# Kernel tuning notes

Hardware: AMD Instinct MI355X
Metric: run time of the kernel (lower is better)

## Reference

```python
import jax, jax.numpy as jnp
import numpy as np

B, N, H, FE, M, PASSES, OUT = 512, 40, 128, 16, 128, 3, 128
NEG = -1e9


def setup_inputs() -> dict:
    key = jax.random.key(0)
    ks = jax.random.split(key, 16)
    am = jax.random.bernoulli(ks[0], 0.1, (B, N, N))
    am = (am | jnp.swapaxes(am, 1, 2)) & (~jnp.eye(N, dtype=bool))[None]
    edges = jax.random.uniform(ks[1], (B, N, N, FE), dtype=jnp.float32) * am[..., None].astype(jnp.float32)
    nodes = jax.random.normal(ks[2], (B, N, H), dtype=jnp.float32)
    s = lambda f: 1.0 / np.sqrt(f)
    return {
        "nodes": nodes,
        "edges": edges,
        "We": jax.random.normal(ks[3], (FE, M), dtype=jnp.float32) * s(FE),
        "Wn": jax.random.normal(ks[4], (H, M), dtype=jnp.float32) * s(H),
        "Wm": jax.random.normal(ks[5], (H, M), dtype=jnp.float32) * s(H),
        "Wi": jax.random.normal(ks[6], (M, 3 * H), dtype=jnp.float32) * s(M),
        "Wh": jax.random.normal(ks[7], (H, 3 * H), dtype=jnp.float32) * s(H),
        "bi": jnp.zeros((3 * H,), jnp.float32),
        "bh": jnp.zeros((3 * H,), jnp.float32),
        "Wg": jax.random.normal(ks[8], (2 * H, OUT), dtype=jnp.float32) * s(2 * H),
        "bg": jnp.zeros((OUT,), jnp.float32),
        "Wo": jax.random.normal(ks[9], (2 * H, OUT), dtype=jnp.float32) * s(2 * H),
        "bo": jnp.zeros((OUT,), jnp.float32),
    }


def _forward(nodes, edges, We, Wn, Wm, Wi, Wh, bi, bh, Wg, bg, Wo, bo):
    adj = jnp.sum(edges, axis=3)                      # (B,N,N)
    nghb_mask = adj > 0                               # neighbor exists
    node_mask = jnp.any(nghb_mask, axis=-1)           # (B,N) node has >=1 neighbor

    h = nodes                                         # hidden == input feature dim
    edge_proj = jnp.einsum("bijf,fm->bijm", edges, We)  # precompute, edges fixed
    for _ in range(PASSES):
        # attention energies over neighbors j of node i (masked softmax)
        nghb_proj = jnp.einsum("bjh,hm->bjm", h, Wn)  # (B,N,M)
        e = jnp.tanh(edge_proj + nghb_proj[:, None, :, :])        # (B,N,N,M)
        e = jnp.where(nghb_mask[..., None], e, NEG)
        att = jax.nn.softmax(e, axis=2)                            # over neighbor axis j
        emb = jnp.einsum("bjh,hm->bjm", h, Wm)                     # (B,N,M)
        messages = jnp.einsum("bijm,bjm->bim", att, emb)           # (B,N,M)
        # GRU cell update (only for existing nodes, as in the node-batch scatter)
        gi = messages @ Wi + bi
        gh = h @ Wh + bh
        r = jax.nn.sigmoid(gi[..., :H] + gh[..., :H])
        z = jax.nn.sigmoid(gi[..., H:2 * H] + gh[..., H:2 * H])
        n = jnp.tanh(gi[..., 2 * H:] + r * gh[..., 2 * H:])
        h_new = (1.0 - z) * n + z * h
        h = jnp.where(node_mask[..., None], h_new, h)

    # gated graph readout over existing nodes
    cat = jnp.concatenate([h, nodes], axis=-1)        # (B,N,2H)
    gate = jax.nn.sigmoid(cat @ Wg + bg)
    emb_out = cat @ Wo + bo
    out = jnp.sum(node_mask[..., None] * gate * emb_out, axis=1)   # (B,OUT)
    return out


def reference(nodes, edges, We, Wn, Wm, Wi, Wh, bi, bh, Wg, bg, Wo, bo):
    return _forward(nodes, edges, We, Wn, Wm, Wi, Wh, bi, bh, Wg, bg, Wo, bo)
```

## Files before the change

kernel.cpp:

```cpp
#include <hip/hip_runtime.h>

#define T 512
constexpr int Bc = 512, Nc = 40, Hc = 128, FEc = 16, Mc = 128, OUTc = 128, NPASS = 3;
constexpr int ROWP = 136;
constexpr int EPOOL = 512;

typedef __attribute__((ext_vector_type(8))) short short8;
typedef __attribute__((ext_vector_type(4))) float floatx4;
typedef __attribute__((ext_vector_type(4))) float fvec4;

constexpr int WS_WN = 0, WS_WM = 16384, WS_WI = 32768, WS_WH = 81920, WS_WG = 131072, WS_WO = 163840;

__device__ __forceinline__ float fast_rcp(float x) { return __builtin_amdgcn_rcpf(x); }
__device__ __forceinline__ float fast_sigmoid(float x) { return fast_rcp(1.f + __expf(-x)); }
__device__ __forceinline__ float fast_tanh(float x) {
    float t = __expf(2.f * x);
    return 1.f - 2.f * fast_rcp(t + 1.f);
}
__device__ __forceinline__ float bf2f(unsigned short u) {
    union { unsigned int i; float f; } v; v.i = ((unsigned int)u) << 16; return v.f;
}
__device__ __forceinline__ unsigned short f2bf(float f) {
    union { float f; unsigned int i; } v; v.f = f;
    unsigned int r = v.i + 0x7fff + ((v.i >> 16) & 1);
    return (unsigned short)(r >> 16);
}
__device__ __forceinline__ float bflo(unsigned int d) {
    union { unsigned int i; float f; } v; v.i = d << 16; return v.f;
}
__device__ __forceinline__ float bfhi(unsigned int d) {
    union { unsigned int i; float f; } v; v.i = d & 0xffff0000u; return v.f;
}

__device__ __forceinline__ floatx4 mm(short8 a, short8 b, floatx4 c) {
    return __builtin_amdgcn_mfma_f32_16x16x32_bf16(a, b, c, 0, 0, 0);
}
__device__ __forceinline__ short8 afrag(const unsigned short* buf, int mt, int kt, int lane) {
    int row = mt * 16 + (lane & 15); row = row > 39 ? 39 : row;
    return *(const short8*)(buf + row * ROWP + kt * 32 + (lane >> 4) * 8);
}
__device__ __forceinline__ short8 bfrag(const unsigned short* w, int nt, int nKT, int kt, int lane) {
    return *(const short8*)(w + ((nt * nKT + kt) * 64 + lane) * 8);
}

__global__ void prep_kernel(const float* __restrict__ Wn, const float* __restrict__ Wm,
                            const float* __restrict__ Wi, const float* __restrict__ Wh,
                            const float* __restrict__ Wg, const float* __restrict__ Wo,
                            unsigned short* __restrict__ ws) {
    int c = blockIdx.x, lane = threadIdx.x;
    int quad = lane >> 4, l16 = lane & 15;
    const float* W; int N, nKT, local; unsigned short* dst;
    if (c < 32)       { W = Wn; N = 128; nKT = 4; local = c;       dst = ws + WS_WN; }
    else if (c < 64)  { W = Wm; N = 128; nKT = 4; local = c - 32;  dst = ws + WS_WM; }
    else if (c < 160) { W = Wi; N = 384; nKT = 4; local = c - 64;  dst = ws + WS_WI; }
    else if (c < 256) { W = Wh; N = 384; nKT = 4; local = c - 160; dst = ws + WS_WH; }
    else if (c < 320) { W = Wg; N = 128; nKT = 8; local = c - 256; dst = ws + WS_WG; }
    else              { W = Wo; N = 128; nKT = 8; local = c - 320; dst = ws + WS_WO; }
    int nt = local / nKT, kt = local % nKT;
    short8 v;
#pragma unroll
    for (int j = 0; j < 8; ++j) {
        int k = kt * 32 + quad * 8 + j;
        v[j] = (short)f2bf(W[k * N + nt * 16 + l16]);
    }
    *(short8*)(dst + local * 512 + lane * 8) = v;
}

__global__ __launch_bounds__(T, 4) void mpnn_kernel(
    const float* __restrict__ nodes, const float* __restrict__ edges,
    const float* __restrict__ We, const float* __restrict__ bi,
    const float* __restrict__ bh, const float* __restrict__ bg,
    const float* __restrict__ bo, const unsigned short* __restrict__ ws,
    float* __restrict__ out)
{
    __shared__ __attribute__((aligned(16))) unsigned short s_hb[Nc * ROWP];
    __shared__ __attribute__((aligned(16))) unsigned short s_mb[Nc * ROWP];
    __shared__ __attribute__((aligned(16))) unsigned short s_npb[Nc * ROWP];
    __shared__ __attribute__((aligned(16))) unsigned short s_eb[Nc * ROWP];
    __shared__ __attribute__((aligned(16))) unsigned short s_pool[EPOOL * FEc];
    __shared__ unsigned char s_nbr[Nc][Nc];
    __shared__ int s_cnt[Nc];
    __shared__ int s_off[Nc];
    __shared__ int s_total;

    const int b = blockIdx.x, tid = threadIdx.x;
    const int lane = tid & 63, wave = tid >> 6;
    const int quad = lane >> 4, l16 = lane & 15;
    const int m = tid & 127, g = tid >> 7;
    const int col = wave * 16 + l16;

    const float* nodes_b = nodes + (size_t)b * Nc * Hc;
    const float* edges_b = edges + (size_t)b * Nc * Nc * FEc;
    const unsigned short* wWn = ws + WS_WN; const unsigned short* wWm = ws + WS_WM;
    const unsigned short* wWi = ws + WS_WI; const unsigned short* wWh = ws + WS_WH;
    const unsigned short* wWg = ws + WS_WG; const unsigned short* wWo = ws + WS_WO;

    float hreg[3][4];
#pragma unroll
    for (int mt = 0; mt < 3; ++mt)
#pragma unroll
        for (int reg = 0; reg < 4; ++reg) {
            int row = mt * 16 + quad * 4 + reg;
            float v = (row < Nc) ? nodes_b[row * Hc + col] : 0.f;
            hreg[mt][reg] = v;
            if (row < Nc) s_hb[row * ROWP + col] = f2bf(v);
        }
    for (int p = tid; p < Nc * Nc; p += T) {
        const fvec4* e4 = (const fvec4*)(edges_b + p * FEc);
        fvec4 a0 = __builtin_nontemporal_load(e4);
        fvec4 a1 = __builtin_nontemporal_load(e4 + 1);
        fvec4 a2 = __builtin_nontemporal_load(e4 + 2);
        fvec4 a3 = __builtin_nontemporal_load(e4 + 3);
        float s = a0.x + a0.y + a0.z + a0.w + a1.x + a1.y + a1.z + a1.w
                + a2.x + a2.y + a2.z + a2.w + a3.x + a3.y + a3.z + a3.w;
        ((unsigned char*)s_nbr)[p] = (s > 0.f) ? 1 : 0;
    }
    __syncthreads();
    if (tid < Nc) {
        int c = 0;
#pragma unroll 1
        for (int j = 0; j < Nc; ++j)
            if (s_nbr[tid][j]) { s_nbr[tid][c] = (unsigned char)j; ++c; }
        s_cnt[tid] = c;
    }
    __syncthreads();
    if (tid == 0) {
        int tot = 0;
#pragma unroll 1
        for (int i = 0; i < Nc; ++i) { s_off[i] = tot; tot += s_cnt[i]; }
        s_total = tot;
    }
    __syncthreads();
    int* slot_src = (int*)s_eb;
    if (tid < Nc) {
        int base = s_off[tid], cnt = s_cnt[tid];
#pragma unroll 1
        for (int kn = 0; kn < cnt; ++kn) {
            int slot = base + kn;
            if (slot < EPOOL) slot_src[slot] = tid * Nc + s_nbr[tid][kn];
        }
    }
    __syncthreads();
    {
        const int E = s_total < EPOOL ? s_total : EPOOL;
#pragma unroll 1
        for (int w = tid; w < E * 2; w += T) {
            int s = w >> 1, hf = w & 1;
            const float* src = edges_b + (size_t)slot_src[s] * FEc + hf * 8;
            fvec4 x = __builtin_nontemporal_load((const fvec4*)src);
            fvec4 y = __builtin_nontemporal_load((const fvec4*)(src + 4));
            short8 v;
            v[0] = (short)f2bf(x.x); v[1] = (short)f2bf(x.y); v[2] = (short)f2bf(x.z); v[3] = (short)f2bf(x.w);
            v[4] = (short)f2bf(y.x); v[5] = (short)f2bf(y.y); v[6] = (short)f2bf(y.z); v[7] = (short)f2bf(y.w);
            *(short8*)(s_pool + s * FEc + hf * 8) = v;
        }
    }
    __syncthreads();

    for (int pass = 0; pass < NPASS; ++pass) {
#pragma unroll 1
        for (int jb = 0; jb < 2; ++jb) {
            const unsigned short* wb = jb ? wWm : wWn;
            unsigned short* dst = jb ? s_eb : s_npb;
            short8 bfr[4];
#pragma unroll
            for (int kt = 0; kt < 4; ++kt) bfr[kt] = bfrag(wb, wave, 4, kt, lane);
#pragma unroll 1
            for (int mt = 0; mt < 3; ++mt) {
                floatx4 acc = {0.f, 0.f, 0.f, 0.f};
#pragma unroll
                for (int kt = 0; kt < 4; ++kt) acc = mm(afrag(s_hb, mt, kt, lane), bfr[kt], acc);
#pragma unroll
                for (int reg = 0; reg < 4; ++reg) {
                    int row = mt * 16 + quad * 4 + reg;
                    if (row < Nc) dst[row * ROWP + col] = f2bf(acc[reg]);
                }
            }
        }
        __syncthreads();

        {
            float wef[FEc];
#pragma unroll
            for (int f = 0; f < FEc; ++f) wef[f] = We[f * Mc + m];
#pragma unroll 1
            for (int ib = 0; ib < 10; ++ib) {
                int i = g + ib * 4;
                int cnt = s_cnt[i], base = s_off[i];
                int cap = EPOOL - base; if (cap > cnt) cap = cnt; if (cap < 0) cap = 0;
                float pden = 0.f, pnum = 0.f;
                int kn = 0;
#pragma unroll 1
                for (; kn < cap; ++kn) {
                    int j = s_nbr[i][kn];
                    const unsigned int* e = (const unsigned int*)(s_pool + (base + kn) * FEc);
                    uint4 p0 = *(const uint4*)e;
                    uint4 p1 = *(const uint4*)(e + 4);
                    float ep = bflo(p0.x)*wef[0]  + bfhi(p0.x)*wef[1]
                             + bflo(p0.y)*wef[2]  + bfhi(p0.y)*wef[3]
                             + bflo(p0.z)*wef[4]  + bfhi(p0.z)*wef[5]
                             + bflo(p0.w)*wef[6]  + bfhi(p0.w)*wef[7]
                             + bflo(p1.x)*wef[8]  + bfhi(p1.x)*wef[9]
                             + bflo(p1.y)*wef[10] + bfhi(p1.y)*wef[11]
                             + bflo(p1.z)*wef[12] + bfhi(p1.z)*wef[13]
                             + bflo(p1.w)*wef[14] + bfhi(p1.w)*wef[15];
                    float w = __expf(fast_tanh(ep + bf2f(s_npb[j * ROWP + m])));
                    pden += w;
                    pnum += w * bf2f(s_eb[j * ROWP + m]);
                }
#pragma unroll 1
                for (; kn < cnt; ++kn) {
                    int j = s_nbr[i][kn];
                    const float4* ef = (const float4*)(edges_b + ((size_t)i * Nc + j) * FEc);
                    float4 a0 = ef[0], a1 = ef[1], a2 = ef[2], a3 = ef[3];
                    float ep = a0.x*wef[0] + a0.y*wef[1] + a0.z*wef[2] + a0.w*wef[3]
                             + a1.x*wef[4] + a1.y*wef[5] + a1.z*wef[6] + a1.w*wef[7]
                             + a2.x*wef[8] + a2.y*wef[9] + a2.z*wef[10]+ a2.w*wef[11]
                             + a3.x*wef[12]+ a3.y*wef[13]+ a3.z*wef[14]+ a3.w*wef[15];
                    float w = __expf(fast_tanh(ep + bf2f(s_npb[j * ROWP + m])));
                    pden += w;
                    pnum += w * bf2f(s_eb[j * ROWP + m]);
                }
                s_mb[i * ROWP + m] = f2bf((cnt > 0) ? pnum * fast_rcp(pden) : 0.f);
            }
        }
        __syncthreads();

#pragma unroll 1
        for (int grp = 0; grp < 2; ++grp) {
            unsigned short* dst = grp ? s_eb : s_npb;
            float bb = bi[grp * 128 + col] + bh[grp * 128 + col];
#pragma unroll 1
            for (int mt = 0; mt < 3; ++mt) {
                floatx4 acc = {0.f,0.f,0.f,0.f};
#pragma unroll 1
                for (int kt = 0; kt < 4; ++kt) {
                    acc = mm(afrag(s_mb, mt, kt, lane), bfrag(wWi, grp * 8 + wave, 4, kt, lane), acc);
                    acc = mm(afrag(s_hb, mt, kt, lane), bfrag(wWh, grp * 8 + wave, 4, kt, lane), acc);
                }
#pragma unroll
                for (int reg = 0; reg < 4; ++reg) {
                    int row = mt * 16 + quad * 4 + reg;
                    if (row < Nc) dst[row * ROWP + col] = f2bf(fast_sigmoid(acc[reg] + bb));
                }
            }
        }
        {
            float bnI = bi[256 + col], bnH = bh[256 + col];
#pragma unroll
            for (int mt = 0; mt < 3; ++mt) {
                floatx4 ai = {0.f,0.f,0.f,0.f}, ah = {0.f,0.f,0.f,0.f};
#pragma unroll 1
                for (int kt = 0; kt < 4; ++kt) {
                    ai = mm(afrag(s_mb, mt, kt, lane), bfrag(wWi, 16 + wave, 4, kt, lane), ai);
                    ah = mm(afrag(s_hb, mt, kt, lane), bfrag(wWh, 16 + wave, 4, kt, lane), ah);
                }
#pragma unroll
                for (int reg = 0; reg < 4; ++reg) {
                    int row = mt * 16 + quad * 4 + reg;
                    if (row < Nc) {
                        float hold = hreg[mt][reg];
                        float r = bf2f(s_npb[row * ROWP + col]);
                        float z = bf2f(s_eb[row * ROWP + col]);
                        float n = fast_tanh(ai[reg] + bnI + r * (ah[reg] + bnH));
                        float v = (1.f - z) * n + z * hold;
                        hreg[mt][reg] = (s_cnt[row] > 0) ? v : hold;
                    }
                }
            }
        }
        __syncthreads();
#pragma unroll
        for (int mt = 0; mt < 3; ++mt)
#pragma unroll
            for (int reg = 0; reg < 4; ++reg) {
                int row = mt * 16 + quad * 4 + reg;
                if (row < Nc) s_hb[row * ROWP + col] = f2bf(hreg[mt][reg]);
            }
        __syncthreads();
    }

    for (int idx = tid; idx < Nc * Hc; idx += T) {
        int row = idx >> 7, c2 = idx & 127;
        s_mb[row * ROWP + c2] = f2bf(nodes_b[idx]);
    }
    __syncthreads();
    float psum = 0.f;
    {
        float bgv = bg[col], bov = bo[col];
#pragma unroll 1
        for (int mt = 0; mt < 3; ++mt) {
            floatx4 ga = {0.f,0.f,0.f,0.f}, oa = {0.f,0.f,0.f,0.f};
#pragma unroll 1
            for (int kt = 0; kt < 8; ++kt) {
                short8 a = (kt < 4) ? afrag(s_hb, mt, kt, lane) : afrag(s_mb, mt, kt - 4, lane);
                ga = mm(a, bfrag(wWg, wave, 8, kt, lane), ga);
                oa = mm(a, bfrag(wWo, wave, 8, kt, lane), oa);
            }
#pragma unroll
            for (int reg = 0; reg < 4; ++reg) {
                int row = mt * 16 + quad * 4 + reg;
                if (row < Nc && s_cnt[row] > 0)
                    psum += fast_sigmoid(ga[reg] + bgv) * (oa[reg] + bov);
            }
        }
    }
    psum += __shfl_xor(psum, 16);
    psum += __shfl_xor(psum, 32);
    if (quad == 0) out[(size_t)b * OUTc + col] = psum;
}

extern "C" void kernel_launch(void* const* d_in, const int* in_sizes, int n_in,
                              void* d_out, int out_size, void* d_ws, size_t ws_size,
                              hipStream_t stream) {
    const float* nodes = (const float*)d_in[0];
    const float* edges = (const float*)d_in[1];
    const float* We = (const float*)d_in[2];
    const float* Wn = (const float*)d_in[3];
    const float* Wm = (const float*)d_in[4];
    const float* Wi = (const float*)d_in[5];
    const float* Wh = (const float*)d_in[6];
    const float* bi = (const float*)d_in[7];
    const float* bh = (const float*)d_in[8];
    const float* Wg = (const float*)d_in[9];
    const float* bg = (const float*)d_in[10];
    const float* Wo = (const float*)d_in[11];
    const float* bo = (const float*)d_in[12];
    float* out = (float*)d_out;
    unsigned short* ws = (unsigned short*)d_ws;

    prep_kernel<<<384, 64, 0, stream>>>(Wn, Wm, Wi, Wh, Wg, Wo, ws);
    mpnn_kernel<<<Bc, T, 0, stream>>>(nodes, edges, We, bi, bh, bg, bo, ws, out);
}
```

Before: 277.3 us.

## Compute edge projections with MFMA in chunks instead of per-lane scalar dot products

The 16-wide edge-feature projection is now computed with bf16 MFMA over chunks of 64 pooled edges and staged in a shared-memory buffer. The attention loop then reads the precomputed projection per edge instead of doing a 16-term scalar FMA per lane per pass. Accumulators for the 10 rows each thread owns are kept in registers across chunks. This adds about 17KB of LDS (which can lower occupancy), two barriers per chunk, and the bf16 rounding of the projection, while removing repeated scalar work across passes.

```diff
diff --git a/kernel.cpp b/kernel.cpp
--- a/kernel.cpp
+++ b/kernel.cpp
@@ -4,12 +4,15 @@
 constexpr int Bc = 512, Nc = 40, Hc = 128, FEc = 16, Mc = 128, OUTc = 128, NPASS = 3;
 constexpr int ROWP = 136;
 constexpr int EPOOL = 512;
+constexpr int EPP = 132;
+constexpr int CH = 64;
 
 typedef __attribute__((ext_vector_type(8))) short short8;
 typedef __attribute__((ext_vector_type(4))) float floatx4;
 typedef __attribute__((ext_vector_type(4))) float fvec4;
 
 constexpr int WS_WN = 0, WS_WM = 16384, WS_WI = 32768, WS_WH = 81920, WS_WG = 131072, WS_WO = 163840;
+constexpr int WS_WE16 = 196608;
 
 __device__ __forceinline__ float fast_rcp(float x) { return __builtin_amdgcn_rcpf(x); }
 __device__ __forceinline__ float fast_sigmoid(float x) { return fast_rcp(1.f + __expf(-x)); }
@@ -25,12 +28,6 @@
     unsigned int r = v.i + 0x7fff + ((v.i >> 16) & 1);
     return (unsigned short)(r >> 16);
 }
-__device__ __forceinline__ float bflo(unsigned int d) {
-    union { unsigned int i; float f; } v; v.i = d << 16; return v.f;
-}
-__device__ __forceinline__ float bfhi(unsigned int d) {
-    union { unsigned int i; float f; } v; v.i = d & 0xffff0000u; return v.f;
-}
 
 __device__ __forceinline__ floatx4 mm(short8 a, short8 b, floatx4 c) {
     return __builtin_amdgcn_mfma_f32_16x16x32_bf16(a, b, c, 0, 0, 0);
@@ -46,9 +43,20 @@
 __global__ void prep_kernel(const float* __restrict__ Wn, const float* __restrict__ Wm,
                             const float* __restrict__ Wi, const float* __restrict__ Wh,
                             const float* __restrict__ Wg, const float* __restrict__ Wo,
-                            unsigned short* __restrict__ ws) {
+                            const float* __restrict__ We, unsigned short* __restrict__ ws) {
     int c = blockIdx.x, lane = threadIdx.x;
     int quad = lane >> 4, l16 = lane & 15;
+    if (c >= 384) {
+        int nt = c - 384;
+        short8 v;
+#pragma unroll
+        for (int j = 0; j < 8; ++j) {
+            int k = quad * 8 + j;
+            v[j] = (k < FEc) ? (short)f2bf(We[k * Mc + nt * 16 + l16]) : (short)0;
+        }
+        *(short8*)(ws + WS_WE16 + nt * 512 + lane * 8) = v;
+        return;
+    }
     const float* W; int N, nKT, local; unsigned short* dst;
     if (c < 32)       { W = Wn; N = 128; nKT = 4; local = c;       dst = ws + WS_WN; }
     else if (c < 64)  { W = Wm; N = 128; nKT = 4; local = c - 32;  dst = ws + WS_WM; }
@@ -77,8 +85,10 @@
     __shared__ __attribute__((aligned(16))) unsigned short s_mb[Nc * ROWP];
     __shared__ __attribute__((aligned(16))) unsigned short s_npb[Nc * ROWP];
     __shared__ __attribute__((aligned(16))) unsigned short s_eb[Nc * ROWP];
-    __shared__ __attribute__((aligned(16))) unsigned short s_pool[EPOOL * FEc];
+    __shared__ __attribute__((aligned(16))) unsigned short s_poolb[EPOOL * FEc];
+    __shared__ __attribute__((aligned(16))) unsigned short s_ep[CH * EPP];
     __shared__ unsigned char s_nbr[Nc][Nc];
+    __shared__ unsigned char s_jof[EPOOL];
     __shared__ int s_cnt[Nc];
     __shared__ int s_off[Nc];
     __shared__ int s_total;
@@ -137,22 +147,28 @@
 #pragma unroll 1
         for (int kn = 0; kn < cnt; ++kn) {
             int slot = base + kn;
-            if (slot < EPOOL) slot_src[slot] = tid * Nc + s_nbr[tid][kn];
+            if (slot < EPOOL) {
+                int j = s_nbr[tid][kn];
+                slot_src[slot] = tid * Nc + j;
+                s_jof[slot] = (unsigned char)j;
+            }
         }
     }
     __syncthreads();
     {
         const int E = s_total < EPOOL ? s_total : EPOOL;
 #pragma unroll 1
-        for (int w = tid; w < E * 2; w += T) {
+        for (int w = tid; w < EPOOL * 2; w += T) {
             int s = w >> 1, hf = w & 1;
-            const float* src = edges_b + (size_t)slot_src[s] * FEc + hf * 8;
-            fvec4 x = __builtin_nontemporal_load((const fvec4*)src);
-            fvec4 y = __builtin_nontemporal_load((const fvec4*)(src + 4));
-            short8 v;
-            v[0] = (short)f2bf(x.x); v[1] = (short)f2bf(x.y); v[2] = (short)f2bf(x.z); v[3] = (short)f2bf(x.w);
-            v[4] = (short)f2bf(y.x); v[5] = (short)f2bf(y.y); v[6] = (short)f2bf(y.z); v[7] = (short)f2bf(y.w);
-            *(short8*)(s_pool + s * FEc + hf * 8) = v;
+            short8 v = {0,0,0,0,0,0,0,0};
+            if (s < E) {
+                const float* src = edges_b + (size_t)slot_src[s] * FEc + hf * 8;
+                fvec4 x = __builtin_nontemporal_load((const fvec4*)src);
+                fvec4 y = __builtin_nontemporal_load((const fvec4*)(src + 4));
+                v[0] = (short)f2bf(x.x); v[1] = (short)f2bf(x.y); v[2] = (short)f2bf(x.z); v[3] = (short)f2bf(x.w);
+                v[4] = (short)f2bf(y.x); v[5] = (short)f2bf(y.y); v[6] = (short)f2bf(y.z); v[7] = (short)f2bf(y.w);
+            }
+            *(short8*)(s_poolb + s * FEc + hf * 8) = v;
         }
     }
     __syncthreads();
@@ -180,48 +196,71 @@
         __syncthreads();
 
         {
-            float wef[FEc];
-#pragma unroll
-            for (int f = 0; f < FEc; ++f) wef[f] = We[f * Mc + m];
-#pragma unroll 1
+            float pd[10], pn[10];
+#pragma unroll
+            for (int ib = 0; ib < 10; ++ib) { pd[ib] = 0.f; pn[ib] = 0.f; }
+            const int E = s_total < EPOOL ? s_total : EPOOL;
+            const int nCh = (E + CH - 1) / CH;
+            short8 bfrW = bfrag(ws + WS_WE16, wave, 1, 0, lane);
+#pragma unroll 1
+            for (int ch = 0; ch < nCh; ++ch) {
+                const int c0 = ch * CH;
+#pragma unroll 1
+                for (int st = 0; st < 4; ++st) {
+                    short8 a = {0,0,0,0,0,0,0,0};
+                    if (quad < 2) {
+                        int slot = c0 + st * 16 + l16;
+                        a = *(const short8*)(s_poolb + slot * FEc + quad * 8);
+                    }
+                    floatx4 acc = {0.f, 0.f, 0.f, 0.f};
+                    acc = mm(a, bfrW, acc);
+#pragma unroll
+                    for (int reg = 0; reg < 4; ++reg) {
+                        int sl = st * 16 + quad * 4 + reg;
+                        s_ep[sl * EPP + col] = f2bf(acc[reg]);
+                    }
+                }
+                __syncthreads();
+                const int c1 = c0 + CH;
+#pragma unroll
+                for (int ib = 0; ib < 10; ++ib) {
+                    int i = g + ib * 4;
+                    int base = __builtin_amdgcn_readfirstlane(s_off[i]);
+                    int cnt  = __builtin_amdgcn_readfirstlane(s_cnt[i]);
+                    int e0 = base > c0 ? base : c0;
+                    int e1 = base + cnt; if (e1 > c1) e1 = c1;
+#pragma unroll 1
+                    for (int s = e0; s < e1; ++s) {
+                        int j = s_jof[s];
+                        float ep = bf2f(s_ep[(s - c0) * EPP + m]);
+                        float x = ep + bf2f(s_npb[j * ROWP + m]);
+                        float w = __expf(fast_tanh(x));
+                        pd[ib] += w;
+                        pn[ib] += w * bf2f(s_eb[j * ROWP + m]);
+                    }
+                }
+                __syncthreads();
+            }
+#pragma unroll
             for (int ib = 0; ib < 10; ++ib) {
                 int i = g + ib * 4;
-                int cnt = s_cnt[i], base = s_off[i];
-                int cap = EPOOL - base; if (cap > cnt) cap = cnt; if (cap < 0) cap = 0;
-                float pden = 0.f, pnum = 0.f;
-                int kn = 0;
-#pragma unroll 1
-                for (; kn < cap; ++kn) {
-                    int j = s_nbr[i][kn];
-                    const unsigned int* e = (const unsigned int*)(s_pool + (base + kn) * FEc);
-                    uint4 p0 = *(const uint4*)e;
-                    uint4 p1 = *(const uint4*)(e + 4);
-                    float ep = bflo(p0.x)*wef[0]  + bfhi(p0.x)*wef[1]
-                             + bflo(p0.y)*wef[2]  + bfhi(p0.y)*wef[3]
-                             + bflo(p0.z)*wef[4]  + bfhi(p0.z)*wef[5]
-                             + bflo(p0.w)*wef[6]  + bfhi(p0.w)*wef[7]
-                             + bflo(p1.x)*wef[8]  + bfhi(p1.x)*wef[9]
-                             + bflo(p1.y)*wef[10] + bfhi(p1.y)*wef[11]
-                             + bflo(p1.z)*wef[12] + bfhi(p1.z)*wef[13]
-                             + bflo(p1.w)*wef[14] + bfhi(p1.w)*wef[15];
-                    float w = __expf(fast_tanh(ep + bf2f(s_npb[j * ROWP + m])));
-                    pden += w;
-                    pnum += w * bf2f(s_eb[j * ROWP + m]);
-                }
-#pragma unroll 1
-                for (; kn < cnt; ++kn) {
+                int base = __builtin_amdgcn_readfirstlane(s_off[i]);
+                int cnt  = __builtin_amdgcn_readfirstlane(s_cnt[i]);
+                int kn0 = EPOOL - base; if (kn0 > cnt) kn0 = cnt; if (kn0 < 0) kn0 = 0;
+#pragma unroll 1
+                for (int kn = kn0; kn < cnt; ++kn) {
                     int j = s_nbr[i][kn];
                     const float4* ef = (const float4*)(edges_b + ((size_t)i * Nc + j) * FEc);
                     float4 a0 = ef[0], a1 = ef[1], a2 = ef[2], a3 = ef[3];
-                    float ep = a0.x*wef[0] + a0.y*wef[1] + a0.z*wef[2] + a0.w*wef[3]
-                             + a1.x*wef[4] + a1.y*wef[5] + a1.z*wef[6] + a1.w*wef[7]
-                             + a2.x*wef[8] + a2.y*wef[9] + a2.z*wef[10]+ a2.w*wef[11]
-                             + a3.x*wef[12]+ a3.y*wef[13]+ a3.z*wef[14]+ a3.w*wef[15];
+                    float ep = a0.x*We[0*Mc+m] + a0.y*We[1*Mc+m] + a0.z*We[2*Mc+m] + a0.w*We[3*Mc+m]
+                             + a1.x*We[4*Mc+m] + a1.y*We[5*Mc+m] + a1.z*We[6*Mc+m] + a1.w*We[7*Mc+m]
+                             + a2.x*We[8*Mc+m] + a2.y*We[9*Mc+m] + a2.z*We[10*Mc+m]+ a2.w*We[11*Mc+m]
+                             + a3.x*We[12*Mc+m]+ a3.y*We[13*Mc+m]+ a3.z*We[14*Mc+m]+ a3.w*We[15*Mc+m];
                     float w = __expf(fast_tanh(ep + bf2f(s_npb[j * ROWP + m])));
-                    pden += w;
-                    pnum += w * bf2f(s_eb[j * ROWP + m]);
-                }
-                s_mb[i * ROWP + m] = f2bf((cnt > 0) ? pnum * fast_rcp(pden) : 0.f);
+                    pd[ib] += w;
+                    pn[ib] += w * bf2f(s_eb[j * ROWP + m]);
+                }
+                s_mb[i * ROWP + m] = f2bf((cnt > 0) ? pn[ib] * fast_rcp(pd[ib]) : 0.f);
             }
         }
         __syncthreads();
@@ -329,6 +368,6 @@
     float* out = (float*)d_out;
     unsigned short* ws = (unsigned short*)d_ws;
 
-    prep_kernel<<<384, 64, 0, stream>>>(Wn, Wm, Wi, Wh, Wg, Wo, ws);
+    prep_kernel<<<392, 64, 0, stream>>>(Wn, Wm, Wi, Wh, Wg, Wo, We, ws);
     mpnn_kernel<<<Bc, T, 0, stream>>>(nodes, edges, We, bi, bh, bg, bo, ws, out);
 }
```

Result: slower. 290.4 us (+4.7%).
